# Kernel optimization log

Measured on AMD Instinct MI355X. Metric: run time of the kernel, lower is better.

## Reference

```python
import jax, jax.numpy as jnp
import numpy as np

NIN, NOUT, ES, HS, NL = 2, 2, 16, 16, 3
B, T = 4096, 512


def setup_inputs() -> dict:
    key = jax.random.key(0)
    ks = jax.random.split(key, 4 + 4 * NL)
    s_in = 1.0 / np.sqrt(NIN)
    s_es = 1.0 / np.sqrt(ES)
    s_hs = 1.0 / np.sqrt(HS)
    inp = {
        'x': jax.random.normal(ks[0], (B, T, NIN), dtype=jnp.float32),
        'h0': jnp.zeros((NL, B, HS), dtype=jnp.float32),
        'W_emb': jax.random.uniform(ks[1], (ES, NIN), minval=-s_in, maxval=s_in, dtype=jnp.float32),
        'b_emb': jnp.zeros((ES,), dtype=jnp.float32),
        'W_out': jax.random.uniform(ks[2], (NOUT, HS), minval=-s_hs, maxval=s_hs, dtype=jnp.float32),
        'b_out': jnp.zeros((NOUT,), dtype=jnp.float32),
    }
    for l in range(NL):
        in_dim = ES if l == 0 else HS
        k0, k1, k2, k3 = jax.random.split(ks[4 + l], 4)
        inp[f'W_ih{l}'] = jax.random.uniform(k0, (3 * HS, in_dim), minval=-s_hs, maxval=s_hs, dtype=jnp.float32)
        inp[f'W_hh{l}'] = jax.random.uniform(k1, (3 * HS, HS), minval=-s_hs, maxval=s_hs, dtype=jnp.float32)
        inp[f'b_ih{l}'] = jax.random.uniform(k2, (3 * HS,), minval=-s_hs, maxval=s_hs, dtype=jnp.float32)
        inp[f'b_hh{l}'] = jax.random.uniform(k3, (3 * HS,), minval=-s_hs, maxval=s_hs, dtype=jnp.float32)
    return inp


def _gru_layer(x_seq, h0, W_ih, b_ih, W_hh, b_hh):
    # Precompute input-side gates for all timesteps: [B, T, 3H]
    gx = jnp.einsum('bti,gi->btg', x_seq, W_ih) + b_ih

    def step(h, gx_t):
        gh = h @ W_hh.T + b_hh  # [B, 3H]
        xr, xz, xn = jnp.split(gx_t, 3, axis=-1)
        hr, hz, hn = jnp.split(gh, 3, axis=-1)
        r = jax.nn.sigmoid(xr + hr)
        z = jax.nn.sigmoid(xz + hz)
        n = jnp.tanh(xn + r * hn)
        h_new = (1.0 - z) * n + z * h
        return h_new, h_new

    hT, ys = jax.lax.scan(step, h0, gx.transpose(1, 0, 2))  # scan over T
    return ys.transpose(1, 0, 2), hT  # [B, T, H], [B, H]


def reference(x, h0, W_emb, b_emb, W_out, b_out,
              W_ih0, W_hh0, b_ih0, b_hh0,
              W_ih1, W_hh1, b_ih1, b_hh1,
              W_ih2, W_hh2, b_ih2, b_hh2):
    # Embedding linear + ReLU
    h = jax.nn.relu(jnp.einsum('bti,ei->bte', x, W_emb) + b_emb)  # [B, T, ES]
    layer_params = [
        (W_ih0, b_ih0, W_hh0, b_hh0),
        (W_ih1, b_ih1, W_hh1, b_hh1),
        (W_ih2, b_ih2, W_hh2, b_hh2),
    ]
    finals = []
    for l, (Wi, bi, Wh, bh) in enumerate(layer_params):
        h, hT = _gru_layer(h, h0[l], Wi, bi, Wh, bh)
        finals.append(hT)
    hidden = jnp.stack(finals, axis=0)  # [NL, B, HS]
    out = jnp.einsum('bth,oh->bto', h, W_out) + b_out  # [B, T, NOUT]
    return out, hidden
```

## Files before the change

kernel.cpp:

```cpp
#include <hip/hip_runtime.h>
#include <hip/hip_bf16.h>

#define TT 512
#define BB 4096

typedef __attribute__((ext_vector_type(4))) float f32x4;
typedef __attribute__((ext_vector_type(8))) short short8;
typedef __attribute__((ext_vector_type(8))) __bf16 bf16v8;

__device__ __forceinline__ f32x4 MFMA(short8 a, short8 b, f32x4 c) {
    return __builtin_amdgcn_mfma_f32_16x16x32_bf16(
        __builtin_bit_cast(bf16v8, a), __builtin_bit_cast(bf16v8, b), c, 0, 0, 0);
}

__device__ __forceinline__ float sigmoid_f(float x) {
    return __builtin_amdgcn_rcpf(1.0f + __expf(-x));
}
__device__ __forceinline__ float tanh_f(float x) {
    return fmaf(2.0f, __builtin_amdgcn_rcpf(1.0f + __expf(-2.0f * x)), -1.0f);
}

__device__ __forceinline__ ushort bfbits(float f) {
    return __bfloat16_as_ushort(__float2bfloat16(f));
}
__device__ __forceinline__ float bf2f(ushort u) {
    return __uint_as_float(((unsigned)u) << 16);
}

__device__ __forceinline__ short8 mk_b(const f32x4& v) {
    short8 B;
#pragma unroll
    for (int q = 0; q < 4; ++q) {
        const short hi = (short)bfbits(v[q]);
        B[2 * q] = hi; B[2 * q + 1] = hi;
    }
    return B;
}

__global__ __launch_bounds__(256, 1)
void gru_pipe4_kernel(const float* __restrict__ x, const float* __restrict__ h0,
                      const float* __restrict__ W_emb, const float* __restrict__ b_emb,
                      const float* __restrict__ W_out, const float* __restrict__ b_out,
                      const float* __restrict__ Wih0, const float* __restrict__ Whh0,
                      const float* __restrict__ bih0, const float* __restrict__ bhh0,
                      const float* __restrict__ Wih1, const float* __restrict__ Whh1,
                      const float* __restrict__ bih1, const float* __restrict__ bhh1,
                      const float* __restrict__ Wih2, const float* __restrict__ Whh2,
                      const float* __restrict__ bih2, const float* __restrict__ bhh2,
                      float* __restrict__ out)
{
    const int tid = threadIdx.x;
    const int wid = tid >> 6;
    const int l   = tid & 63;
    const int n   = l & 15;
    const int g   = l >> 4;
    const int b   = blockIdx.x * 16 + n;

    __shared__ short8 lbuf[2][2][4][64];
    __shared__ f32x4  obuf[2][4][64];

    const int lw = wid < 3 ? wid : 2;
    const float* Wih = lw == 0 ? Wih0 : (lw == 1 ? Wih1 : Wih2);
    const float* Whh = lw == 0 ? Whh0 : (lw == 1 ? Whh1 : Whh2);
    const float* bih = lw == 0 ? bih0 : (lw == 1 ? bih1 : bih2);
    const float* bhh = lw == 0 ? bhh0 : (lw == 1 ? bhh1 : bhh2);

    short8 aW[2][3];
#pragma unroll
    for (int sd = 0; sd < 2; ++sd) {
        const float* W = sd ? Whh : Wih;
#pragma unroll
        for (int gate = 0; gate < 3; ++gate) {
            short8 f;
#pragma unroll
            for (int q = 0; q < 4; ++q) {
                const float w = W[(gate * 16 + n) * 16 + (4 * g + q)];
                const ushort hi = bfbits(w);
                const ushort lo = bfbits(w - bf2f(hi));
                f[2 * q] = (short)hi; f[2 * q + 1] = (short)lo;
            }
            aW[sd][gate] = f;
        }
    }

    f32x4 bR, bZ, bNX, bNH;
#pragma unroll
    for (int j = 0; j < 4; ++j) {
        const int m = 4 * g + j;
        bR[j]  = bih[m]      + bhh[m];
        bZ[j]  = bih[16 + m] + bhh[16 + m];
        bNX[j] = bih[32 + m];
        bNH[j] = bhh[32 + m];
    }

    float wex[4], wey[4], beq[4];
#pragma unroll
    for (int q = 0; q < 4; ++q) {
        const int c = 4 * g + q;
        wex[q] = W_emb[c * 2]; wey[q] = W_emb[c * 2 + 1]; beq[q] = b_emb[c];
    }
    float wo0[4], wo1[4];
#pragma unroll
    for (int j = 0; j < 4; ++j) { wo0[j] = W_out[4 * g + j]; wo1[j] = W_out[16 + 4 * g + j]; }
    const float bo0 = b_out[0], bo1 = b_out[1];

    f32x4 hC = *(const f32x4*)(h0 + ((size_t)lw * BB + b) * 16 + 4 * g);
    short8 hB = mk_b(hC);

    const float* xb = x + (size_t)b * (TT * 2);
    float4 xc0 = make_float4(0.f, 0.f, 0.f, 0.f), xc1 = xc0;
    if (wid == 0) { xc0 = *(const float4*)xb; xc1 = *(const float4*)(xb + 4); }

#define GATES(AR, AZ, ANH, ANX)                                         \
    do {                                                                \
        _Pragma("unroll")                                               \
        for (int j = 0; j < 4; ++j) {                                   \
            const float r = sigmoid_f(AR[j]);                           \
            const float z = sigmoid_f(AZ[j]);                           \
            const float nn = tanh_f(fmaf(r, ANH[j], ANX[j]));           \
            hC[j] = fmaf(z, hC[j] - nn, nn);                            \
        }                                                               \
        hB = mk_b(hC);                                                  \
    } while (0)

#define HANDOFF(i)                                                      \
    do {                                                                \
        if (wid < 2) lbuf[s & 1][wid][i][l] = hB;                       \
        else         obuf[s & 1][i][l] = hC;                            \
    } while (0)

    const int NS = TT / 4 + 3;
    for (int s = 0; s < NS; ++s) {
        const int t0 = 4 * (s - wid);
        if (t0 >= 0 && t0 < TT) {
            if (wid < 3) {
                short8 inB0, inB1, inB2, inB3;
                if (wid == 0) {
                    f32x4 e0, e1, e2, e3;
#pragma unroll
                    for (int q = 0; q < 4; ++q) {
                        e0[q] = fmaxf(fmaf(wey[q], xc0.y, fmaf(wex[q], xc0.x, beq[q])), 0.0f);
                        e1[q] = fmaxf(fmaf(wey[q], xc0.w, fmaf(wex[q], xc0.z, beq[q])), 0.0f);
                        e2[q] = fmaxf(fmaf(wey[q], xc1.y, fmaf(wex[q], xc1.x, beq[q])), 0.0f);
                        e3[q] = fmaxf(fmaf(wey[q], xc1.w, fmaf(wex[q], xc1.z, beq[q])), 0.0f);
                    }
                    inB0 = mk_b(e0); inB1 = mk_b(e1); inB2 = mk_b(e2); inB3 = mk_b(e3);
                    if (t0 + 4 < TT) {
                        xc0 = *(const float4*)(xb + (t0 + 4) * 2);
                        xc1 = *(const float4*)(xb + (t0 + 4) * 2 + 4);
                    }
                } else {
                    const int pp = (s - 1) & 1;
                    inB0 = lbuf[pp][wid - 1][0][l];
                    inB1 = lbuf[pp][wid - 1][1][l];
                    inB2 = lbuf[pp][wid - 1][2][l];
                    inB3 = lbuf[pp][wid - 1][3][l];
                }

                f32x4 arA  = MFMA(aW[1][0], hB, bR);
                f32x4 azA  = MFMA(aW[1][1], hB, bZ);
                f32x4 anhA = MFMA(aW[1][2], hB, bNH);
                f32x4 anxA = MFMA(aW[0][2], inB0, bNX);
                arA = MFMA(aW[0][0], inB0, arA);
                azA = MFMA(aW[0][1], inB0, azA);
                f32x4 arB  = MFMA(aW[0][0], inB1, bR);
                f32x4 azB  = MFMA(aW[0][1], inB1, bZ);
                f32x4 anxB = MFMA(aW[0][2], inB1, bNX);
                GATES(arA, azA, anhA, anxA);
                HANDOFF(0);
                f32x4 anhB = MFMA(aW[1][2], hB, bNH);
                arB = MFMA(aW[1][0], hB, arB);
                azB = MFMA(aW[1][1], hB, azB);
                arA  = MFMA(aW[0][0], inB2, bR);
                azA  = MFMA(aW[0][1], inB2, bZ);
                anxA = MFMA(aW[0][2], inB2, bNX);
                GATES(arB, azB, anhB, anxB);
                HANDOFF(1);
                anhA = MFMA(aW[1][2], hB, bNH);
                arA = MFMA(aW[1][0], hB, arA);
                azA = MFMA(aW[1][1], hB, azA);
                arB  = MFMA(aW[0][0], inB3, bR);
                azB  = MFMA(aW[0][1], inB3, bZ);
                anxB = MFMA(aW[0][2], inB3, bNX);
                GATES(arA, azA, anhA, anxA);
                HANDOFF(2);
                anhB = MFMA(aW[1][2], hB, bNH);
                arB = MFMA(aW[1][0], hB, arB);
                azB = MFMA(aW[1][1], hB, azB);
                GATES(arB, azB, anhB, anxB);
                HANDOFF(3);
            } else {
                const int pp = (s - 1) & 1;
                float p[8];
#pragma unroll
                for (int i = 0; i < 4; ++i) {
                    const f32x4 h2 = obuf[pp][i][l];
                    float p0 = 0.f, p1 = 0.f;
#pragma unroll
                    for (int j = 0; j < 4; ++j) {
                        p0 = fmaf(wo0[j], h2[j], p0);
                        p1 = fmaf(wo1[j], h2[j], p1);
                    }
                    p0 += __shfl_xor(p0, 16); p0 += __shfl_xor(p0, 32);
                    p1 += __shfl_xor(p1, 16); p1 += __shfl_xor(p1, 32);
                    p[2 * i] = p0 + bo0; p[2 * i + 1] = p1 + bo1;
                }
                if (g == 0) {
                    float* op = out + (size_t)b * (TT * 2) + t0 * 2;
                    *(float4*)(op)     = make_float4(p[0], p[1], p[2], p[3]);
                    *(float4*)(op + 4) = make_float4(p[4], p[5], p[6], p[7]);
                }
            }
        }
        asm volatile("s_waitcnt lgkmcnt(0)\n\ts_barrier" ::: "memory");
    }

    if (wid < 3)
        *(f32x4*)(out + (size_t)BB * TT * 2 + ((size_t)wid * BB + b) * 16 + 4 * g) = hC;

#undef GATES
#undef HANDOFF
}

extern "C" void kernel_launch(void* const* d_in, const int* in_sizes, int n_in,
                              void* d_out, int out_size, void* d_ws, size_t ws_size,
                              hipStream_t stream) {
    const float* x     = (const float*)d_in[0];
    const float* h0    = (const float*)d_in[1];
    const float* W_emb = (const float*)d_in[2];
    const float* b_emb = (const float*)d_in[3];
    const float* W_out = (const float*)d_in[4];
    const float* b_out = (const float*)d_in[5];
    const float* Wih0  = (const float*)d_in[6];
    const float* Whh0  = (const float*)d_in[7];
    const float* bih0  = (const float*)d_in[8];
    const float* bhh0  = (const float*)d_in[9];
    const float* Wih1  = (const float*)d_in[10];
    const float* Whh1  = (const float*)d_in[11];
    const float* bih1  = (const float*)d_in[12];
    const float* bhh1  = (const float*)d_in[13];
    const float* Wih2  = (const float*)d_in[14];
    const float* Whh2  = (const float*)d_in[15];
    const float* bih2  = (const float*)d_in[16];
    const float* bhh2  = (const float*)d_in[17];
    float* out = (float*)d_out;

    gru_pipe4_kernel<<<dim3(BB / 16), dim3(256), 0, stream>>>(
        x, h0, W_emb, b_emb, W_out, b_out,
        Wih0, Whh0, bih0, bhh0,
        Wih1, Whh1, bih1, bhh1,
        Wih2, Whh2, bih2, bhh2,
        out);
}
```

Measured before the change: 192.3 us.

## Pack two batch pipelines per block and fold exp2 scaling into weights

Each block now runs two independent 4-wave layer pipelines (512 threads, 32 batch rows), which halves the grid to 128 blocks. The per-step barrier is shared by all eight waves, and more waves are available to interleave MFMA and transcendental latency. The gate weights and biases are pre-scaled by -log2(e) or -2*log2(e), so sigmoid and tanh use exp2f directly and skip a multiply on the recurrent critical path. With 256 CUs, 128 blocks may leave half the device idle, and the shared barrier couples the two pipelines.

```diff
diff --git a/kernel.cpp b/kernel.cpp
--- a/kernel.cpp
+++ b/kernel.cpp
@@ -13,12 +13,7 @@
         __builtin_bit_cast(bf16v8, a), __builtin_bit_cast(bf16v8, b), c, 0, 0, 0);
 }
 
-__device__ __forceinline__ float sigmoid_f(float x) {
-    return __builtin_amdgcn_rcpf(1.0f + __expf(-x));
-}
-__device__ __forceinline__ float tanh_f(float x) {
-    return fmaf(2.0f, __builtin_amdgcn_rcpf(1.0f + __expf(-2.0f * x)), -1.0f);
-}
+__device__ __forceinline__ float fast_rcp(float x) { return __builtin_amdgcn_rcpf(x); }
 
 __device__ __forceinline__ ushort bfbits(float f) {
     return __bfloat16_as_ushort(__float2bfloat16(f));
@@ -37,27 +32,31 @@
     return B;
 }
 
-__global__ __launch_bounds__(256, 1)
-void gru_pipe4_kernel(const float* __restrict__ x, const float* __restrict__ h0,
-                      const float* __restrict__ W_emb, const float* __restrict__ b_emb,
-                      const float* __restrict__ W_out, const float* __restrict__ b_out,
-                      const float* __restrict__ Wih0, const float* __restrict__ Whh0,
-                      const float* __restrict__ bih0, const float* __restrict__ bhh0,
-                      const float* __restrict__ Wih1, const float* __restrict__ Whh1,
-                      const float* __restrict__ bih1, const float* __restrict__ bhh1,
-                      const float* __restrict__ Wih2, const float* __restrict__ Whh2,
-                      const float* __restrict__ bih2, const float* __restrict__ bhh2,
-                      float* __restrict__ out)
+#define KS1 (-1.44269504088896340736f)
+#define KS2 (-2.88539008177792681472f)
+
+__global__ __launch_bounds__(512, 1)
+void gru_pipe4x2_kernel(const float* __restrict__ x, const float* __restrict__ h0,
+                        const float* __restrict__ W_emb, const float* __restrict__ b_emb,
+                        const float* __restrict__ W_out, const float* __restrict__ b_out,
+                        const float* __restrict__ Wih0, const float* __restrict__ Whh0,
+                        const float* __restrict__ bih0, const float* __restrict__ bhh0,
+                        const float* __restrict__ Wih1, const float* __restrict__ Whh1,
+                        const float* __restrict__ bih1, const float* __restrict__ bhh1,
+                        const float* __restrict__ Wih2, const float* __restrict__ Whh2,
+                        const float* __restrict__ bih2, const float* __restrict__ bhh2,
+                        float* __restrict__ out)
 {
     const int tid = threadIdx.x;
-    const int wid = tid >> 6;
+    const int p   = tid >> 8;
+    const int wid = (tid >> 6) & 3;
     const int l   = tid & 63;
     const int n   = l & 15;
     const int g   = l >> 4;
-    const int b   = blockIdx.x * 16 + n;
-
-    __shared__ short8 lbuf[2][2][4][64];
-    __shared__ f32x4  obuf[2][4][64];
+    const int b   = blockIdx.x * 32 + p * 16 + n;
+
+    __shared__ short8 lbuf[2][2][2][4][64];
+    __shared__ f32x4  obuf[2][2][4][64];
 
     const int lw = wid < 3 ? wid : 2;
     const float* Wih = lw == 0 ? Wih0 : (lw == 1 ? Wih1 : Wih2);
@@ -71,10 +70,11 @@
         const float* W = sd ? Whh : Wih;
 #pragma unroll
         for (int gate = 0; gate < 3; ++gate) {
+            const float scale = gate == 2 ? KS2 : KS1;
             short8 f;
 #pragma unroll
             for (int q = 0; q < 4; ++q) {
-                const float w = W[(gate * 16 + n) * 16 + (4 * g + q)];
+                const float w = scale * W[(gate * 16 + n) * 16 + (4 * g + q)];
                 const ushort hi = bfbits(w);
                 const ushort lo = bfbits(w - bf2f(hi));
                 f[2 * q] = (short)hi; f[2 * q + 1] = (short)lo;
@@ -87,10 +87,10 @@
 #pragma unroll
     for (int j = 0; j < 4; ++j) {
         const int m = 4 * g + j;
-        bR[j]  = bih[m]      + bhh[m];
-        bZ[j]  = bih[16 + m] + bhh[16 + m];
-        bNX[j] = bih[32 + m];
-        bNH[j] = bhh[32 + m];
+        bR[j]  = KS1 * (bih[m]      + bhh[m]);
+        bZ[j]  = KS1 * (bih[16 + m] + bhh[16 + m]);
+        bNX[j] = KS2 * bih[32 + m];
+        bNH[j] = KS2 * bhh[32 + m];
     }
 
     float wex[4], wey[4], beq[4];
@@ -115,9 +115,10 @@
     do {                                                                \
         _Pragma("unroll")                                               \
         for (int j = 0; j < 4; ++j) {                                   \
-            const float r = sigmoid_f(AR[j]);                           \
-            const float z = sigmoid_f(AZ[j]);                           \
-            const float nn = tanh_f(fmaf(r, ANH[j], ANX[j]));           \
+            const float r = fast_rcp(1.0f + exp2f(AR[j]));              \
+            const float z = fast_rcp(1.0f + exp2f(AZ[j]));              \
+            const float En = exp2f(fmaf(r, ANH[j], ANX[j]));            \
+            const float nn = fmaf(2.0f, fast_rcp(1.0f + En), -1.0f);    \
             hC[j] = fmaf(z, hC[j] - nn, nn);                            \
         }                                                               \
         hB = mk_b(hC);                                                  \
@@ -125,8 +126,8 @@
 
 #define HANDOFF(i)                                                      \
     do {                                                                \
-        if (wid < 2) lbuf[s & 1][wid][i][l] = hB;                       \
-        else         obuf[s & 1][i][l] = hC;                            \
+        if (wid < 2) lbuf[p][s & 1][wid][i][l] = hB;                    \
+        else         obuf[p][s & 1][i][l] = hC;                         \
     } while (0)
 
     const int NS = TT / 4 + 3;
@@ -151,10 +152,10 @@
                     }
                 } else {
                     const int pp = (s - 1) & 1;
-                    inB0 = lbuf[pp][wid - 1][0][l];
-                    inB1 = lbuf[pp][wid - 1][1][l];
-                    inB2 = lbuf[pp][wid - 1][2][l];
-                    inB3 = lbuf[pp][wid - 1][3][l];
+                    inB0 = lbuf[p][pp][wid - 1][0][l];
+                    inB1 = lbuf[p][pp][wid - 1][1][l];
+                    inB2 = lbuf[p][pp][wid - 1][2][l];
+                    inB3 = lbuf[p][pp][wid - 1][3][l];
                 }
 
                 f32x4 arA  = MFMA(aW[1][0], hB, bR);
@@ -191,10 +192,10 @@
                 HANDOFF(3);
             } else {
                 const int pp = (s - 1) & 1;
-                float p[8];
+                float pr[8];
 #pragma unroll
                 for (int i = 0; i < 4; ++i) {
-                    const f32x4 h2 = obuf[pp][i][l];
+                    const f32x4 h2 = obuf[p][pp][i][l];
                     float p0 = 0.f, p1 = 0.f;
 #pragma unroll
                     for (int j = 0; j < 4; ++j) {
@@ -203,12 +204,12 @@
                     }
                     p0 += __shfl_xor(p0, 16); p0 += __shfl_xor(p0, 32);
                     p1 += __shfl_xor(p1, 16); p1 += __shfl_xor(p1, 32);
-                    p[2 * i] = p0 + bo0; p[2 * i + 1] = p1 + bo1;
+                    pr[2 * i] = p0 + bo0; pr[2 * i + 1] = p1 + bo1;
                 }
                 if (g == 0) {
                     float* op = out + (size_t)b * (TT * 2) + t0 * 2;
-                    *(float4*)(op)     = make_float4(p[0], p[1], p[2], p[3]);
-                    *(float4*)(op + 4) = make_float4(p[4], p[5], p[6], p[7]);
+                    *(float4*)(op)     = make_float4(pr[0], pr[1], pr[2], pr[3]);
+                    *(float4*)(op + 4) = make_float4(pr[4], pr[5], pr[6], pr[7]);
                 }
             }
         }
@@ -245,7 +246,7 @@
     const float* bhh2  = (const float*)d_in[17];
     float* out = (float*)d_out;
 
-    gru_pipe4_kernel<<<dim3(BB / 16), dim3(256), 0, stream>>>(
+    gru_pipe4x2_kernel<<<dim3(BB / 32), dim3(512), 0, stream>>>(
         x, h0, W_emb, b_emb, W_out, b_out,
         Wih0, Whh0, bih0, bhh0,
         Wih1, Whh1, bih1, bhh1,
```

Result: slower. 360.1 us (+87.3%).
